# Kernel optimization log

Hardware: AMD Instinct MI355X
Metric: run time of the kernel (lower is better)

Reference implementation:

```python
import jax, jax.numpy as jnp
import numpy as np

B, S, D = 1, 4096, 768
H = 12
HD = D // H  # 64


def setup_inputs() -> dict:
    key = jax.random.key(0)
    ks = jax.random.split(key, 6)
    sc = 1.0 / np.sqrt(D)
    return {
        "x": jax.random.normal(ks[0], (B, S, D), dtype=jnp.float32),
        "wq": jax.random.normal(ks[1], (D, D), dtype=jnp.float32) * sc,
        "wk": jax.random.normal(ks[2], (D, D), dtype=jnp.float32) * sc,
        "wv": jax.random.normal(ks[3], (D, D), dtype=jnp.float32) * sc,
        "wo": jax.random.normal(ks[4], (D, D), dtype=jnp.float32) * sc,
        "bo": jax.random.normal(ks[5], (D,), dtype=jnp.float32) * 0.02,
    }


def reference(x, wq, wk, wv, wo, bo):
    b, n, _ = x.shape
    # projections (torch Linear: x @ W.T; here weights stored as (d_in, d_out))
    q = (x @ wq).reshape(b, n, H, HD).transpose(0, 2, 1, 3)  # b h n d
    k = (x @ wk).reshape(b, n, H, HD).transpose(0, 2, 1, 3)
    v = (x @ wv).reshape(b, n, H, HD).transpose(0, 2, 1, 3)
    scores = jnp.einsum("bhqd,bhkd->bhqk", q, k)
    causal = jnp.tril(jnp.ones((n, n), dtype=bool))  # True = keep
    scores = jnp.where(causal, scores, -jnp.inf)
    weights = jax.nn.softmax(scores / np.sqrt(HD), axis=-1)
    ctx = jnp.einsum("bhqk,bhkd->bhqd", weights, v)
    ctx = ctx.transpose(0, 2, 1, 3).reshape(b, n, D)
    return ctx @ wo + bo
```

## Files before the change

### kernel.cpp

```cpp
#include <hip/hip_runtime.h>


typedef short bf16x8 __attribute__((ext_vector_type(8)));
typedef float f32x4 __attribute__((ext_vector_type(4)));
typedef unsigned short u16;

static constexpr int S_LEN = 4096;
static constexpr int DIM   = 768;
static constexpr int NH    = 12;
static constexpr float QSCALE = 0.125f * 1.44269504088896340736f;

__device__ inline u16 f2bf(float f) {
  union { float f; unsigned int u; } v; v.f = f;
  unsigned int r = v.u + 0x7FFFu + ((v.u >> 16) & 1u);
  return (u16)(r >> 16);
}

__device__ inline void gload_lds16(const u16* g, u16* s) {
  __builtin_amdgcn_global_load_lds(
      (const __attribute__((address_space(1))) unsigned int*)g,
      (__attribute__((address_space(3))) unsigned int*)s, 16, 0, 0);
}

__global__ __launch_bounds__(256)
void prep_kernel(const float* __restrict__ x, const float* __restrict__ w0,
                 const float* __restrict__ w1, const float* __restrict__ w2,
                 const float* __restrict__ w3, u16* __restrict__ xb,
                 u16* __restrict__ t0, u16* __restrict__ t1,
                 u16* __restrict__ t2, u16* __restrict__ t3) {
  if (blockIdx.z == 4) {
    const size_t n = (size_t)S_LEN * DIM;
    const int id = blockIdx.y * 12 + blockIdx.x;
    const size_t stride = (size_t)144 * 256 * 8;
    for (size_t i = ((size_t)id * 256 + threadIdx.x) * 8; i < n; i += stride) {
      const float4 a = *(const float4*)(x + i);
      const float4 b = *(const float4*)(x + i + 4);
      bf16x8 o;
      o[0] = (short)f2bf(a.x); o[1] = (short)f2bf(a.y);
      o[2] = (short)f2bf(a.z); o[3] = (short)f2bf(a.w);
      o[4] = (short)f2bf(b.x); o[5] = (short)f2bf(b.y);
      o[6] = (short)f2bf(b.z); o[7] = (short)f2bf(b.w);
      *(bf16x8*)(xb + i) = o;
    }
    return;
  }
  __shared__ float T[64][65];
  const float* src; u16* dst;
  switch (blockIdx.z) {
    case 0: src = w0; dst = t0; break;
    case 1: src = w1; dst = t1; break;
    case 2: src = w2; dst = t2; break;
    default: src = w3; dst = t3; break;
  }
  const int k0 = blockIdx.y * 64, n0 = blockIdx.x * 64;
  const int r = threadIdx.x >> 2, c0 = (threadIdx.x & 3) * 16;
#pragma unroll
  for (int i = 0; i < 4; ++i) {
    const float4 v = *(const float4*)(src + (size_t)(k0 + r) * DIM + n0 + c0 + i * 4);
    T[r][c0 + i * 4 + 0] = v.x;
    T[r][c0 + i * 4 + 1] = v.y;
    T[r][c0 + i * 4 + 2] = v.z;
    T[r][c0 + i * 4 + 3] = v.w;
  }
  __syncthreads();
  bf16x8 o0, o1;
#pragma unroll
  for (int i = 0; i < 8; ++i) {
    o0[i] = (short)f2bf(T[c0 + i][r]);
    o1[i] = (short)f2bf(T[c0 + 8 + i][r]);
  }
  *(bf16x8*)(dst + (size_t)(n0 + r) * DIM + k0 + c0) = o0;
  *(bf16x8*)(dst + (size_t)(n0 + r) * DIM + k0 + c0 + 8) = o1;
}

template <int MODE>
__global__ __launch_bounds__(256)
void mfma_gemm_kernel(const u16* __restrict__ A, const u16* __restrict__ Bq,
                      const u16* __restrict__ Bk, const u16* __restrict__ Bv,
                      const float* __restrict__ bias, u16* __restrict__ Qb,
                      u16* __restrict__ Kb, u16* __restrict__ VT,
                      float* __restrict__ Out) {
  constexpr int MT = (MODE == 0) ? 4 : 2;
  constexpr int BM = MT * 32;
  __shared__ __align__(16) u16 Al[BM * 64];
  __shared__ __align__(16) u16 Bl[96 * 64];

  const int tid  = threadIdx.x;
  const int wv   = tid >> 6;
  const int lane = tid & 63;
  const int quad = lane >> 4;
  const int l16  = lane & 15;
  const int wr = wv >> 1, wc = wv & 1;
  const int m0 = blockIdx.y * BM;
  const int n0 = blockIdx.x * 96;

  int wi = 0, nb = n0;
  const u16* BT = Bq;
  if (MODE == 0) {
    wi = n0 / DIM;
    nb = n0 - wi * DIM;
    BT = (wi == 0) ? Bq : (wi == 1) ? Bk : Bv;
  }

  const int sr8 = lane >> 3;
  const int sc  = ((lane & 7) ^ sr8) * 8;
  const int key = l16 & 7;

  const bool swp = (MODE == 1) || (wi < 2);

  f32x4 acc[MT][3] = {};

  for (int k0 = 0; k0 < DIM; k0 += 64) {
    __syncthreads();
#pragma unroll
    for (int j = 0; j < MT; ++j)
      gload_lds16(A + (size_t)(m0 + wv * (BM / 4) + j * 8 + sr8) * DIM + k0 + sc,
                  &Al[(wv * (BM / 4) + j * 8) * 64]);
#pragma unroll
    for (int j = 0; j < 3; ++j)
      gload_lds16(BT + (size_t)(nb + wv * 24 + j * 8 + sr8) * DIM + k0 + sc,
                  &Bl[(wv * 24 + j * 8) * 64]);
    __syncthreads();

#pragma unroll
    for (int kh = 0; kh < 2; ++kh) {
      const int cb = kh * 4;
      bf16x8 af[MT], bfr[3];
#pragma unroll
      for (int mt = 0; mt < MT; ++mt) {
        const int row = wr * (BM / 2) + mt * 16 + l16;
        af[mt] = *(const bf16x8*)&Al[row * 64 + ((cb + quad) ^ key) * 8];
      }
#pragma unroll
      for (int nt = 0; nt < 3; ++nt) {
        const int row = wc * 48 + nt * 16 + l16;
        bfr[nt] = *(const bf16x8*)&Bl[row * 64 + ((cb + quad) ^ key) * 8];
      }
      if (swp) {
#pragma unroll
        for (int mt = 0; mt < MT; ++mt)
#pragma unroll
          for (int nt = 0; nt < 3; ++nt)
            acc[mt][nt] = __builtin_amdgcn_mfma_f32_16x16x32_bf16(
                bfr[nt], af[mt], acc[mt][nt], 0, 0, 0);
      } else {
#pragma unroll
        for (int mt = 0; mt < MT; ++mt)
#pragma unroll
          for (int nt = 0; nt < 3; ++nt)
            acc[mt][nt] = __builtin_amdgcn_mfma_f32_16x16x32_bf16(
                af[mt], bfr[nt], acc[mt][nt], 0, 0, 0);
      }
    }
  }

  if (MODE == 0 && wi >= 2) {
#pragma unroll
    for (int mt = 0; mt < MT; ++mt) {
#pragma unroll
      for (int nt = 0; nt < 3; ++nt) {
        const int row  = m0 + wr * (BM / 2) + mt * 16 + quad * 4;
        const int ncol = nb + wc * 48 + nt * 16 + l16;
        u16 pk[4];
#pragma unroll
        for (int r = 0; r < 4; ++r) pk[r] = f2bf(acc[mt][nt][r]);
        unsigned long long v;
        __builtin_memcpy(&v, pk, 8);
        *(unsigned long long*)(VT + (size_t)ncol * S_LEN + row) = v;
      }
    }
  } else if (MODE == 0) {
    u16* dst = (wi == 0) ? Qb : Kb;
    const float sc_out = (wi == 0) ? QSCALE : 1.0f;
#pragma unroll
    for (int mt = 0; mt < MT; ++mt) {
#pragma unroll
      for (int nt = 0; nt < 3; ++nt) {
        const int row = m0 + wr * (BM / 2) + mt * 16 + l16;
        const int ncb = nb + wc * 48 + nt * 16 + quad * 4;
        u16 pk[4];
#pragma unroll
        for (int r = 0; r < 4; ++r) pk[r] = f2bf(acc[mt][nt][r] * sc_out);
        unsigned long long v;
        __builtin_memcpy(&v, pk, 8);
        *(unsigned long long*)(dst + (size_t)row * DIM + ncb) = v;
      }
    }
  } else {
#pragma unroll
    for (int mt = 0; mt < MT; ++mt) {
#pragma unroll
      for (int nt = 0; nt < 3; ++nt) {
        const int row = m0 + wr * (BM / 2) + mt * 16 + l16;
        const int ncb = n0 + wc * 48 + nt * 16 + quad * 4;
        const float4 b4 = *(const float4*)(bias + ncb);
        float4 ov;
        ov.x = acc[mt][nt][0] + b4.x;
        ov.y = acc[mt][nt][1] + b4.y;
        ov.z = acc[mt][nt][2] + b4.z;
        ov.w = acc[mt][nt][3] + b4.w;
        *(float4*)(Out + (size_t)row * DIM + ncb) = ov;
      }
    }
  }
}

__global__ __launch_bounds__(256)
void attn_mfma_kernel(const u16* __restrict__ Qb, const u16* __restrict__ Kb,
                      const u16* __restrict__ VTb, u16* __restrict__ ctx) {
  __shared__ __align__(16) u16 KVl[128 * 64 + 64 * 128];
  __shared__ __align__(16) u16 Pl[4][16 * 72];
  __shared__ float4 lbuf[4][64];

  u16* Kl = KVl;
  u16* Vl = KVl + 128 * 64;

  const int tid  = threadIdx.x;
  const int w    = tid >> 6;
  const int lane = tid & 63;
  const int quad = lane >> 4;
  const int l16  = lane & 15;
  const int qw   = w >> 1;
  const int kw   = w & 1;
  const int key  = l16 & 7;

  const int id = blockIdx.x;
  const int rc = id & 7, slot = id >> 3;
  const int h  = (slot < 64) ? rc : 8 + (rc >> 1);
  const int bx = (slot < 64) ? slot : ((rc & 1) * 32 + (slot - 64));

  const int sr8  = lane >> 3;
  const int scK  = ((lane & 7) ^ sr8) * 8;
  const int sr16 = lane >> 4;

#pragma unroll 1
  for (int side = 0; side < 2; ++side) {
    const int qt = side ? (127 - bx) : bx;
    const int q0 = qt * 32;

    const u16* qptr = Qb + (size_t)(q0 + qw * 16 + l16) * DIM + h * 64 + quad * 8;
    const bf16x8 aq0 = *(const bf16x8*)(qptr);
    const bf16x8 aq1 = *(const bf16x8*)(qptr + 32);

    f32x4 o[4] = {};
    float l_r[4] = {};

    const int nkt = qt / 2 + 1;
    const int niter = (nkt + 1) >> 1;
    const int my_last = nkt - 1;

#pragma unroll 1
    for (int i = 0; i < niter; ++i) {
      const int k0g = i * 128;
      __syncthreads();
#pragma unroll
      for (int j = 0; j < 4; ++j)
        gload_lds16(Kb + (size_t)(k0g + w * 32 + j * 8 + sr8) * DIM + h * 64 + scK,
                    &Kl[(w * 32 + j * 8) * 64]);
#pragma unroll
      for (int j = 0; j < 4; ++j) {
        const int vrow = w * 16 + j * 4 + sr16;
        const int vcol = ((lane & 15) ^ (vrow & 7)) * 8;
        gload_lds16(VTb + (size_t)(h * 64 + vrow) * S_LEN + k0g + vcol,
                    &Vl[(w * 16 + j * 4) * 128]);
      }
      __syncthreads();

      const int kt_w = 2 * i + kw;
      if (kt_w < nkt) {
        f32x4 s[4];
#pragma unroll
        for (int t = 0; t < 4; ++t) {
          const int row = kw * 64 + t * 16 + l16;
          const bf16x8 bk0 = *(const bf16x8*)&Kl[row * 64 + (quad ^ key) * 8];
          const bf16x8 bk1 = *(const bf16x8*)&Kl[row * 64 + ((quad ^ 4) ^ key) * 8];
          s[t] = __builtin_amdgcn_mfma_f32_16x16x32_bf16(
              aq0, bk0, f32x4{0.f, 0.f, 0.f, 0.f}, 0, 0, 0);
          s[t] = __builtin_amdgcn_mfma_f32_16x16x32_bf16(aq1, bk1, s[t], 0, 0, 0);
        }

        if (kt_w == my_last) {
#pragma unroll
          for (int t = 0; t < 4; ++t)
#pragma unroll
            for (int r = 0; r < 4; ++r) {
              const int kvg = k0g + kw * 64 + t * 16 + l16;
              const int qg  = q0 + qw * 16 + quad * 4 + r;
              float p = __builtin_amdgcn_exp2f(s[t][r]);
              if (kvg > qg) p = 0.f;
              l_r[r] += p;
              Pl[w][(quad * 4 + r) * 72 + t * 16 + l16] =
                  (u16)((__float_as_uint(p) + 0x8000u) >> 16);
            }
        } else {
#pragma unroll
          for (int t = 0; t < 4; ++t)
#pragma unroll
            for (int r = 0; r < 4; ++r) {
              const float p = __builtin_amdgcn_exp2f(s[t][r]);
              l_r[r] += p;
              Pl[w][(quad * 4 + r) * 72 + t * 16 + l16] =
                  (u16)((__float_as_uint(p) + 0x8000u) >> 16);
            }
        }

        const bf16x8 pa0 = *(const bf16x8*)&Pl[w][l16 * 72 + quad * 8];
        const bf16x8 pa1 = *(const bf16x8*)&Pl[w][l16 * 72 + 32 + quad * 8];
#pragma unroll
        for (int t = 0; t < 4; ++t) {
          const int row = t * 16 + l16;
          const int c0 = (kw * 8 + quad) ^ key;
          const int c1 = (kw * 8 + quad + 4) ^ key;
          const bf16x8 vb0 = *(const bf16x8*)&Vl[row * 128 + c0 * 8];
          const bf16x8 vb1 = *(const bf16x8*)&Vl[row * 128 + c1 * 8];
          o[t] = __builtin_amdgcn_mfma_f32_16x16x32_bf16(pa0, vb0, o[t], 0, 0, 0);
          o[t] = __builtin_amdgcn_mfma_f32_16x16x32_bf16(pa1, vb1, o[t], 0, 0, 0);
        }
      }
    }

    __syncthreads();
    float* Obuf = (float*)KVl;
#pragma unroll
    for (int t = 0; t < 4; ++t)
      *(f32x4*)&Obuf[(w * 64 + lane) * 20 + t * 4] = o[t];
    lbuf[w][lane] = float4{l_r[0], l_r[1], l_r[2], l_r[3]};
    __syncthreads();
#pragma unroll
    for (int t = 0; t < 4; ++t) {
      const f32x4 po = *(const f32x4*)&Obuf[((w ^ 1) * 64 + lane) * 20 + t * 4];
      o[t] += po;
    }
    {
      const float4 pl = lbuf[w ^ 1][lane];
      l_r[0] += pl.x; l_r[1] += pl.y; l_r[2] += pl.z; l_r[3] += pl.w;
    }

    if (kw == 0) {
#pragma unroll
      for (int r = 0; r < 4; ++r) {
        float l = l_r[r];
        l += __shfl_xor(l, 1);
        l += __shfl_xor(l, 2);
        l += __shfl_xor(l, 4);
        l += __shfl_xor(l, 8);
        const float inv = 1.f / l;
        const int row = q0 + qw * 16 + quad * 4 + r;
#pragma unroll
        for (int t = 0; t < 4; ++t)
          ctx[(size_t)row * DIM + h * 64 + t * 16 + l16] = f2bf(o[t][r] * inv);
      }
    }
  }
}

extern "C" void kernel_launch(void* const* d_in, const int* in_sizes, int n_in,
                              void* d_out, int out_size, void* d_ws,
                              size_t ws_size, hipStream_t stream) {
  const float* x  = (const float*)d_in[0];
  const float* wq = (const float*)d_in[1];
  const float* wk = (const float*)d_in[2];
  const float* wv = (const float*)d_in[3];
  const float* wo = (const float*)d_in[4];
  const float* bo = (const float*)d_in[5];

  const size_t n_x = (size_t)S_LEN * DIM;
  const size_t n_w = (size_t)DIM * DIM;
  u16* xb  = (u16*)d_ws;
  u16* wtq = xb + n_x;
  u16* wtk = wtq + n_w;
  u16* wtv = wtk + n_w;
  u16* wto = wtv + n_w;
  u16* Qb  = wto + n_w;
  u16* Kb  = Qb + n_x;
  u16* VTb = Kb + n_x;
  u16* ctx = VTb + n_x;

  prep_kernel<<<dim3(12, 12, 5), 256, 0, stream>>>(
      x, wq, wk, wv, wo, xb, wtq, wtk, wtv, wto);

  mfma_gemm_kernel<0><<<dim3(24, 32), 256, 0, stream>>>(
      xb, wtq, wtk, wtv, nullptr, Qb, Kb, VTb, nullptr);

  attn_mfma_kernel<<<dim3(768), 256, 0, stream>>>(Qb, Kb, VTb, ctx);

  mfma_gemm_kernel<1><<<dim3(8, 64), 256, 0, stream>>>(
      ctx, wto, nullptr, nullptr, bo, nullptr, nullptr, nullptr, (float*)d_out);
}
```

Measured before the change: 173.2 us.

## Keep softmax probabilities in registers via transposed QK MFMA and permlane swaps

```diff
diff --git a/kernel.cpp b/kernel.cpp
--- a/kernel.cpp
+++ b/kernel.cpp
@@ -209,8 +209,6 @@
 void attn_mfma_kernel(const u16* __restrict__ Qb, const u16* __restrict__ Kb,
                       const u16* __restrict__ VTb, u16* __restrict__ ctx) {
   __shared__ __align__(16) u16 KVl[128 * 64 + 64 * 128];
-  __shared__ __align__(16) u16 Pl[4][16 * 72];
-  __shared__ float4 lbuf[4][64];
 
   u16* Kl = KVl;
   u16* Vl = KVl + 128 * 64;
@@ -243,7 +241,8 @@
     const bf16x8 aq1 = *(const bf16x8*)(qptr + 32);
 
     f32x4 o[4] = {};
-    float l_r[4] = {};
+    float l_s = 0.f;
+    const int qg = q0 + qw * 16 + l16;
 
     const int nkt = qt / 2 + 1;
     const int niter = (nkt + 1) >> 1;
@@ -275,44 +274,70 @@
           const bf16x8 bk0 = *(const bf16x8*)&Kl[row * 64 + (quad ^ key) * 8];
           const bf16x8 bk1 = *(const bf16x8*)&Kl[row * 64 + ((quad ^ 4) ^ key) * 8];
           s[t] = __builtin_amdgcn_mfma_f32_16x16x32_bf16(
-              aq0, bk0, f32x4{0.f, 0.f, 0.f, 0.f}, 0, 0, 0);
-          s[t] = __builtin_amdgcn_mfma_f32_16x16x32_bf16(aq1, bk1, s[t], 0, 0, 0);
+              bk0, aq0, f32x4{0.f, 0.f, 0.f, 0.f}, 0, 0, 0);
+          s[t] = __builtin_amdgcn_mfma_f32_16x16x32_bf16(bk1, aq1, s[t], 0, 0, 0);
         }
 
+        unsigned Wt[4][2];
         if (kt_w == my_last) {
 #pragma unroll
-          for (int t = 0; t < 4; ++t)
+          for (int t = 0; t < 4; ++t) {
+            float pr[4];
 #pragma unroll
             for (int r = 0; r < 4; ++r) {
-              const int kvg = k0g + kw * 64 + t * 16 + l16;
-              const int qg  = q0 + qw * 16 + quad * 4 + r;
+              const int kvg = k0g + kw * 64 + t * 16 + quad * 4 + r;
               float p = __builtin_amdgcn_exp2f(s[t][r]);
               if (kvg > qg) p = 0.f;
-              l_r[r] += p;
-              Pl[w][(quad * 4 + r) * 72 + t * 16 + l16] =
-                  (u16)((__float_as_uint(p) + 0x8000u) >> 16);
+              l_s += p;
+              pr[r] = p;
             }
+            asm("v_cvt_pk_bf16_f32 %0, %1, %2" : "=v"(Wt[t][0]) : "v"(pr[0]), "v"(pr[1]));
+            asm("v_cvt_pk_bf16_f32 %0, %1, %2" : "=v"(Wt[t][1]) : "v"(pr[2]), "v"(pr[3]));
+          }
         } else {
 #pragma unroll
-          for (int t = 0; t < 4; ++t)
+          for (int t = 0; t < 4; ++t) {
+            float pr[4];
 #pragma unroll
             for (int r = 0; r < 4; ++r) {
               const float p = __builtin_amdgcn_exp2f(s[t][r]);
-              l_r[r] += p;
-              Pl[w][(quad * 4 + r) * 72 + t * 16 + l16] =
-                  (u16)((__float_as_uint(p) + 0x8000u) >> 16);
+              l_s += p;
+              pr[r] = p;
             }
+            asm("v_cvt_pk_bf16_f32 %0, %1, %2" : "=v"(Wt[t][0]) : "v"(pr[0]), "v"(pr[1]));
+            asm("v_cvt_pk_bf16_f32 %0, %1, %2" : "=v"(Wt[t][1]) : "v"(pr[2]), "v"(pr[3]));
+          }
         }
 
-        const bf16x8 pa0 = *(const bf16x8*)&Pl[w][l16 * 72 + quad * 8];
-        const bf16x8 pa1 = *(const bf16x8*)&Pl[w][l16 * 72 + 32 + quad * 8];
+        bf16x8 pa0, pa1;
+        {
+          unsigned a0 = Wt[0][0], b0 = Wt[1][0];
+          unsigned a1 = Wt[0][1], b1 = Wt[1][1];
+          asm("v_permlane32_swap_b32 %0, %1" : "+v"(a0), "+v"(b0));
+          asm("v_permlane16_swap_b32 %0, %1" : "+v"(a0), "+v"(b0));
+          asm("v_permlane32_swap_b32 %0, %1" : "+v"(a1), "+v"(b1));
+          asm("v_permlane16_swap_b32 %0, %1" : "+v"(a1), "+v"(b1));
+          union { unsigned u[4]; bf16x8 v; } U0;
+          U0.u[0] = a0; U0.u[1] = a1; U0.u[2] = b0; U0.u[3] = b1;
+          pa0 = U0.v;
+          unsigned c0 = Wt[2][0], d0 = Wt[3][0];
+          unsigned c1 = Wt[2][1], d1 = Wt[3][1];
+          asm("v_permlane32_swap_b32 %0, %1" : "+v"(c0), "+v"(d0));
+          asm("v_permlane16_swap_b32 %0, %1" : "+v"(c0), "+v"(d0));
+          asm("v_permlane32_swap_b32 %0, %1" : "+v"(c1), "+v"(d1));
+          asm("v_permlane16_swap_b32 %0, %1" : "+v"(c1), "+v"(d1));
+          union { unsigned u[4]; bf16x8 v; } U1;
+          U1.u[0] = c0; U1.u[1] = c1; U1.u[2] = d0; U1.u[3] = d1;
+          pa1 = U1.v;
+        }
+
 #pragma unroll
         for (int t = 0; t < 4; ++t) {
           const int row = t * 16 + l16;
-          const int c0 = (kw * 8 + quad) ^ key;
-          const int c1 = (kw * 8 + quad + 4) ^ key;
-          const bf16x8 vb0 = *(const bf16x8*)&Vl[row * 128 + c0 * 8];
-          const bf16x8 vb1 = *(const bf16x8*)&Vl[row * 128 + c1 * 8];
+          const int cc0 = (kw * 8 + quad) ^ key;
+          const int cc1 = (kw * 8 + quad + 4) ^ key;
+          const bf16x8 vb0 = *(const bf16x8*)&Vl[row * 128 + cc0 * 8];
+          const bf16x8 vb1 = *(const bf16x8*)&Vl[row * 128 + cc1 * 8];
           o[t] = __builtin_amdgcn_mfma_f32_16x16x32_bf16(pa0, vb0, o[t], 0, 0, 0);
           o[t] = __builtin_amdgcn_mfma_f32_16x16x32_bf16(pa1, vb1, o[t], 0, 0, 0);
         }
@@ -320,31 +345,27 @@
     }
 
     __syncthreads();
-    float* Obuf = (float*)KVl;
+    float* Obuf  = (float*)KVl;
+    float* lbufF = Obuf + 5120;
 #pragma unroll
     for (int t = 0; t < 4; ++t)
       *(f32x4*)&Obuf[(w * 64 + lane) * 20 + t * 4] = o[t];
-    lbuf[w][lane] = float4{l_r[0], l_r[1], l_r[2], l_r[3]};
+    lbufF[w * 64 + lane] = l_s;
     __syncthreads();
 #pragma unroll
     for (int t = 0; t < 4; ++t) {
       const f32x4 po = *(const f32x4*)&Obuf[((w ^ 1) * 64 + lane) * 20 + t * 4];
       o[t] += po;
     }
-    {
-      const float4 pl = lbuf[w ^ 1][lane];
-      l_r[0] += pl.x; l_r[1] += pl.y; l_r[2] += pl.z; l_r[3] += pl.w;
-    }
+    l_s += lbufF[(w ^ 1) * 64 + lane];
 
     if (kw == 0) {
+      float L = l_s;
+      L += __shfl_xor(L, 16);
+      L += __shfl_xor(L, 32);
 #pragma unroll
       for (int r = 0; r < 4; ++r) {
-        float l = l_r[r];
-        l += __shfl_xor(l, 1);
-        l += __shfl_xor(l, 2);
-        l += __shfl_xor(l, 4);
-        l += __shfl_xor(l, 8);
-        const float inv = 1.f / l;
+        const float inv = 1.f / __shfl(L, quad * 4 + r);
         const int row = q0 + qw * 16 + quad * 4 + r;
 #pragma unroll
         for (int t = 0; t < 4; ++t)
```

New measurement: 169.1 us. -2.4%, faster.
